# Kernel optimization log

Measured on AMD Instinct MI355X. Metric: run time of the kernel, lower is better.

## Reference

```python
import jax, jax.numpy as jnp
import numpy as np

IN_DIM = 512
HID = 1024
E = 16
TOPK = 2


def setup_inputs() -> dict:
    key = jax.random.key(0)
    ks = jax.random.split(key, 8)
    s = 0.02
    x = jax.random.normal(ks[0], (4, 2048, IN_DIM), dtype=jnp.float32)
    Wr = jax.random.normal(ks[1], (IN_DIM, E), dtype=jnp.float32) * s
    br = jnp.zeros((E,), dtype=jnp.float32)
    W1 = jax.random.normal(ks[2], (E, IN_DIM, HID), dtype=jnp.float32) * s
    b1 = jnp.zeros((E, HID), dtype=jnp.float32)
    W2 = jax.random.normal(ks[3], (E, HID, IN_DIM), dtype=jnp.float32) * s
    b2 = jnp.zeros((E, IN_DIM), dtype=jnp.float32)
    return {"x": x, "Wr": Wr, "br": br, "W1": W1, "b1": b1, "W2": W2, "b2": b2}


def reference(x, Wr, br, W1, b1, W2, b2):
    token_shape = x.shape[:-1]
    xf = x.reshape(-1, x.shape[-1])            # [T, D]
    T = xf.shape[0]

    # router (temperature = 1.0)
    logits = xf @ Wr + br                       # [T, E]
    probs = jax.nn.softmax(logits, axis=-1)
    topk_w, topk_idx = jax.lax.top_k(probs, TOPK)           # [T, K]
    topk_w = topk_w / jnp.maximum(topk_w.sum(-1, keepdims=True), 1e-9)

    # combine weights: [T, E], zero where not routed
    combine = jnp.zeros((T, E), dtype=xf.dtype).at[
        jnp.arange(T)[:, None], topk_idx].add(topk_w)

    # per-expert MLP (exact GELU, as torch nn.GELU default), weighted combine
    y = jnp.zeros_like(xf)
    for e in range(E):
        h = jax.nn.gelu(xf @ W1[e] + b1[e], approximate=False)  # [T, H]
        o = h @ W2[e] + b2[e]                                   # [T, D]
        y = y + combine[:, e:e + 1] * o

    # residual (in_dim == out_dim)
    y = xf + y
    return y.reshape(*token_shape, IN_DIM)
```

## Files before the change

### kernel.cpp

```cpp
#include <hip/hip_runtime.h>
#include <hip/hip_bf16.h>
#include <math.h>

#define IN_DIM 512
#define HID    1024
#define NE     16
#define T_TOK  8192
#define NPAIR  (T_TOK*2)

typedef __attribute__((ext_vector_type(8))) short bf16x8;
typedef __attribute__((ext_vector_type(4))) float f32x4;

__device__ __forceinline__ unsigned short f2b(float f){
  unsigned u = __float_as_uint(f);
  u += 0x7FFF + ((u >> 16) & 1);
  return (unsigned short)(u >> 16);
}
__device__ __forceinline__ float b2f(unsigned short u){
  return __uint_as_float(((unsigned)u) << 16);
}

__device__ __forceinline__ void barrier_lds_only(){
  asm volatile("s_waitcnt lgkmcnt(0)" ::: "memory");
  __builtin_amdgcn_s_barrier();
}

__global__ __launch_bounds__(256) void tconv_kernel(const float* __restrict__ in,
                                                    unsigned short* __restrict__ out,
                                                    int M, int N){
  __shared__ float tile[32][33];
  int e  = blockIdx.z;
  int m0 = blockIdx.y*32, n0 = blockIdx.x*32;
  const float* src = in + (size_t)e*M*N;
  unsigned short* dst = out + (size_t)e*M*N;
  int c = threadIdx.x & 31, r = threadIdx.x >> 5;
  #pragma unroll
  for (int i=0;i<4;i++)
    tile[r + i*8][c] = src[(size_t)(m0 + r + i*8)*N + n0 + c];
  __syncthreads();
  int tr  = threadIdx.x >> 3;
  int tc4 = (threadIdx.x & 7) * 4;
  ushort4 o;
  o.x = f2b(tile[tc4+0][tr]); o.y = f2b(tile[tc4+1][tr]);
  o.z = f2b(tile[tc4+2][tr]); o.w = f2b(tile[tc4+3][tr]);
  *(ushort4*)(&dst[(size_t)(n0 + tr)*M + m0 + tc4]) = o;
}

__global__ __launch_bounds__(256) void router_kernel(
    const float* __restrict__ x, const float* __restrict__ Wr, const float* __restrict__ br,
    unsigned short* __restrict__ xb, int* __restrict__ eid, float* __restrict__ pw)
{
  int wid = threadIdx.x >> 6, lane = threadIdx.x & 63;
  int t = blockIdx.x*4 + wid;
  const float4* xr4 = (const float4*)(x + (size_t)t*IN_DIM);
  ushort4*      xb4 = (ushort4*)(xb + (size_t)t*IN_DIM);

  float acc[NE];
  #pragma unroll
  for (int i=0;i<NE;i++) acc[i]=0.f;

  #pragma unroll
  for (int j=0;j<2;j++){
    int f = j*64 + lane;
    float4 v = xr4[f];
    ushort4 o; o.x=f2b(v.x); o.y=f2b(v.y); o.z=f2b(v.z); o.w=f2b(v.w);
    xb4[f] = o;
    const float4* wr4 = (const float4*)(Wr + (size_t)(f*4)*NE);
    const float* vv = (const float*)&v;
    #pragma unroll
    for (int rr=0; rr<4; rr++){
      float xv = vv[rr];
      #pragma unroll
      for (int q=0;q<4;q++){
        float4 w = wr4[rr*4+q];
        acc[q*4+0] += xv*w.x; acc[q*4+1] += xv*w.y;
        acc[q*4+2] += xv*w.z; acc[q*4+3] += xv*w.w;
      }
    }
  }
  #pragma unroll
  for (int off=32; off>=1; off>>=1){
    #pragma unroll
    for (int i=0;i<NE;i++) acc[i] += __shfl_xor(acc[i], off, 64);
  }
  if (lane==0){
    #pragma unroll
    for (int i=0;i<NE;i++) acc[i] += br[i];
    int e0=0; float l0=acc[0];
    #pragma unroll
    for (int i=1;i<NE;i++) if (acc[i] > l0){ l0=acc[i]; e0=i; }
    int e1=-1; float l1=-3.0e38f;
    #pragma unroll
    for (int i=0;i<NE;i++) if (i!=e0 && acc[i] > l1){ l1=acc[i]; e1=i; }
    float w0 = 1.f/(1.f + __expf(l1 - l0));
    float w1 = 1.f - w0;
    pw[t*2+0] = w0; pw[t*2+1] = w1;
    eid[t*2+0] = e0; eid[t*2+1] = e1;
  }
}

__global__ __launch_bounds__(1024) void bucket_kernel(const int* __restrict__ eid,
                                                      int* __restrict__ cnt,
                                                      int* __restrict__ bucket){
  int e = blockIdx.x;
  __shared__ int lbase;
  if (threadIdx.x == 0) lbase = 0;
  __syncthreads();
  int lane = threadIdx.x & 63, wid = threadIdx.x >> 6;
  int* be = bucket + e*T_TOK;
  for (int c = wid*64; c < NPAIR; c += 1024){
    int p = c + lane;
    bool ok = (eid[p] == e);
    unsigned long long m = __ballot(ok);
    int rank = __popcll(m & ((1ull << lane) - 1ull));
    int count = __popcll(m);
    int base = 0;
    if (lane == 0) base = atomicAdd(&lbase, count);
    base = __shfl(base, 0, 64);
    if (ok) be[base + rank] = p;
  }
  __syncthreads();
  if (threadIdx.x == 0) cnt[e] = lbase;
}

template<int KDIM, int NDIM, bool FIRST>
__global__ __launch_bounds__(256) void moe_gemm(
    const unsigned short* __restrict__ A,
    const unsigned short* __restrict__ Bm,
    const float* __restrict__ bias,
    const int* __restrict__ cnt,
    const int* __restrict__ bucket,
    const float* __restrict__ pw,
    unsigned short* __restrict__ hb,
    unsigned short* __restrict__ opb)
{
  constexpr int NS  = KDIM / 32;
  constexpr int NBT = NDIM / 128;

  int ntiles = 0;
  #pragma unroll
  for (int j=0;j<NE;j++) ntiles += ((cnt[j]+63)>>6)*NBT;

  __shared__ unsigned short As[2*64*32];
  __shared__ unsigned short Bs[2*128*32];

  int tid = threadIdx.x;
  int lane = tid & 63, wid = tid >> 6;
  int wm = (wid>>1)*32, wn = (wid&1)*64;
  int lr0 = tid >> 2;
  int c   = tid & 3;
  int sc  = (c ^ ((lr0 >> 1) & 3)) * 8;
  int wA  = lr0*32 + sc;
  int fr = lane & 15, fb = lane >> 4;
  int pf8 = (fb ^ ((fr >> 1) & 3)) * 8;
  int fq = (lane>>4)*4;

  for (int t = blockIdx.x; t < ntiles; t += gridDim.x){
    int e=0, tloc=0, ebase=0, ce=0, itl=1;
    {
      int cum=0, crow=0;
      #pragma unroll
      for (int j=0;j<NE;j++){
        int cj = cnt[j];
        int it = (cj+63)>>6;
        int tj = it * NBT;
        bool in = (t >= cum) & (t < cum+tj);
        if (in){ e=j; tloc=t-cum; ebase=crow; ce=cj; itl=it; }
        cum += tj; crow += cj;
      }
    }
    int i0 = (tloc % itl) * 64;
    int n0 = (tloc / itl) * 128;

    const int* buck = bucket + e*T_TOK;
    int posA = i0 + lr0;
    int arow;
    if (FIRST){
      int pair = (posA < ce) ? buck[posA] : buck[i0];
      arow = pair >> 1;
    } else {
      arow = ebase + posA;
      if (arow > NPAIR-1) arow = NPAIR-1;
    }
    const unsigned short* Ag = A + (size_t)arow*KDIM + c*8;
    const unsigned short* Bg = Bm + (size_t)e*NDIM*KDIM + (size_t)(n0 + lr0)*KDIM + c*8;

    f32x4 acc[2][4];
    #pragma unroll
    for (int a=0;a<2;a++)
      #pragma unroll
      for (int b=0;b<4;b++)
        #pragma unroll
        for (int j=0;j<4;j++) acc[a][b][j] = 0.f;

    float4 ar, br0, br1;
    ar  = *(const float4*)(Ag);
    br0 = *(const float4*)(Bg);
    br1 = *(const float4*)(Bg + (size_t)64*KDIM);
    *(float4*)(As + wA) = ar;
    *(float4*)(Bs + wA) = br0;
    *(float4*)(Bs + wA + 64*32) = br1;
    ar  = *(const float4*)(Ag + 32);
    br0 = *(const float4*)(Bg + 32);
    br1 = *(const float4*)(Bg + (size_t)64*KDIM + 32);
    barrier_lds_only();

    #pragma unroll 2
    for (int k = 0; k < NS; k++){
      const int cur = k & 1, nxt = cur ^ 1;
      float4 na, nb0, nb1;
      bool ld = (k + 2 < NS);
      if (ld){
        na  = *(const float4*)(Ag + (k+2)*32);
        nb0 = *(const float4*)(Bg + (k+2)*32);
        nb1 = *(const float4*)(Bg + (size_t)64*KDIM + (k+2)*32);
      }
      if (k + 1 < NS){
        *(float4*)(As + nxt*2048 + wA) = ar;
        *(float4*)(Bs + nxt*4096 + wA) = br0;
        *(float4*)(Bs + nxt*4096 + wA + 64*32) = br1;
      }
      if (ld){ ar = na; br0 = nb0; br1 = nb1; }

      const unsigned short* Ac = As + cur*2048;
      const unsigned short* Bc = Bs + cur*4096;
      bf16x8 af[2], bfr[4];
      #pragma unroll
      for (int s=0;s<2;s++) af[s]  = *(const bf16x8*)(Ac + (wm + s*16 + fr)*32 + pf8);
      #pragma unroll
      for (int u=0;u<4;u++) bfr[u] = *(const bf16x8*)(Bc + (wn + u*16 + fr)*32 + pf8);
      #pragma unroll
      for (int s=0;s<2;s++)
        #pragma unroll
        for (int u=0;u<4;u++)
          acc[s][u] = __builtin_amdgcn_mfma_f32_16x16x32_bf16(af[s], bfr[u], acc[s][u], 0,0,0);
      barrier_lds_only();
    }

    #pragma unroll
    for (int s=0;s<2;s++){
      #pragma unroll
      for (int i=0;i<4;i++){
        int row = wm + s*16 + fq + i;
        int pos = i0 + row;
        if (pos >= ce) continue;
        #pragma unroll
        for (int u=0;u<4;u++){
          int n = n0 + wn + u*16 + fr;
          float v = acc[s][u][i] + bias[e*NDIM + n];
          if (FIRST){
            float g = 0.5f*v*(1.f + erff(v*0.70710678118654752f));
            hb[(size_t)(ebase + pos)*NDIM + n] = f2b(g);
          } else {
            int pair = buck[pos];
            opb[(size_t)pair*NDIM + n] = f2b(pw[pair]*v);
          }
        }
      }
    }
  }
}

__global__ __launch_bounds__(256) void combine_kernel(const float* __restrict__ x,
                                                      const unsigned short* __restrict__ opb,
                                                      float* __restrict__ out){
  int i = blockIdx.x*256 + threadIdx.x;
  int t  = i >> 7;
  int c4 = i & 127;
  float4 v = ((const float4*)x)[i];
  ushort4 a = ((const ushort4*)opb)[(size_t)(2*t)*128 + c4];
  ushort4 b = ((const ushort4*)opb)[(size_t)(2*t+1)*128 + c4];
  v.x += b2f(a.x) + b2f(b.x);
  v.y += b2f(a.y) + b2f(b.y);
  v.z += b2f(a.z) + b2f(b.z);
  v.w += b2f(a.w) + b2f(b.w);
  ((float4*)out)[i] = v;
}

extern "C" void kernel_launch(void* const* d_in, const int* in_sizes, int n_in,
                              void* d_out, int out_size, void* d_ws, size_t ws_size,
                              hipStream_t stream)
{
  const float* x  = (const float*)d_in[0];
  const float* Wr = (const float*)d_in[1];
  const float* br = (const float*)d_in[2];
  const float* W1 = (const float*)d_in[3];
  const float* b1 = (const float*)d_in[4];
  const float* W2 = (const float*)d_in[5];
  const float* b2 = (const float*)d_in[6];
  float* out = (float*)d_out;
  char* ws = (char*)d_ws;

  int*            cnt    = (int*)(ws + 0);
  int*            bucket = (int*)(ws + 1024);
  float*          pw     = (float*)(ws + 525312);
  unsigned short* xb     = (unsigned short*)(ws + 590848);
  unsigned short* w1t    = (unsigned short*)(ws + 8979456);
  unsigned short* w2t    = (unsigned short*)(ws + 25756672);
  unsigned short* hb     = (unsigned short*)(ws + 42533888);
  int*            eid    = (int*)(ws + 42533888);
  unsigned short* opb    = w1t;

  router_kernel<<<T_TOK/4, 256, 0, stream>>>(x, Wr, br, xb, eid, pw);
  bucket_kernel<<<NE, 1024, 0, stream>>>(eid, cnt, bucket);
  tconv_kernel<<<dim3(HID/32, IN_DIM/32, NE), 256, 0, stream>>>(W1, w1t, IN_DIM, HID);
  tconv_kernel<<<dim3(IN_DIM/32, HID/32, NE), 256, 0, stream>>>(W2, w2t, HID, IN_DIM);
  moe_gemm<IN_DIM, HID, true ><<<1024, 256, 0, stream>>>(
      xb, w1t, b1, cnt, bucket, pw, hb, opb);
  moe_gemm<HID, IN_DIM, false><<<1024, 256, 0, stream>>>(
      hb, w2t, b2, cnt, bucket, pw, hb, opb);
  combine_kernel<<<(T_TOK*IN_DIM/4)/256, 256, 0, stream>>>(x, opb, out);
}
```

Baseline: 281.3 us.

## Enlarge MoE GEMM tiles to 128x128 with direct global-to-LDS loads

```diff
diff --git a/kernel.cpp b/kernel.cpp
--- a/kernel.cpp
+++ b/kernel.cpp
@@ -25,14 +25,31 @@
   __builtin_amdgcn_s_barrier();
 }
 
-__global__ __launch_bounds__(256) void tconv_kernel(const float* __restrict__ in,
-                                                    unsigned short* __restrict__ out,
-                                                    int M, int N){
+typedef const __attribute__((address_space(1))) unsigned int* gas1_t;
+typedef __attribute__((address_space(3))) unsigned int* las3_t;
+__device__ __forceinline__ void gl16(const unsigned short* g, unsigned short* l){
+  __builtin_amdgcn_global_load_lds((gas1_t)(const void*)g, (las3_t)(void*)l, 16, 0, 0);
+}
+
+__global__ __launch_bounds__(256) void tconv2_kernel(const float* __restrict__ A1,
+                                                     unsigned short* __restrict__ O1,
+                                                     const float* __restrict__ A2,
+                                                     unsigned short* __restrict__ O2){
   __shared__ float tile[32][33];
-  int e  = blockIdx.z;
-  int m0 = blockIdx.y*32, n0 = blockIdx.x*32;
-  const float* src = in + (size_t)e*M*N;
-  unsigned short* dst = out + (size_t)e*M*N;
+  int b = blockIdx.x;
+  const float* src; unsigned short* dst; int M, N, m0, n0;
+  if (b < 8192){
+    M = IN_DIM; N = HID;
+    int e = b >> 9, r = b & 511;
+    n0 = (r & 31)*32; m0 = (r >> 5)*32;
+    src = A1 + (size_t)e*M*N; dst = O1 + (size_t)e*M*N;
+  } else {
+    int b2 = b - 8192;
+    M = HID; N = IN_DIM;
+    int e = b2 >> 9, r = b2 & 511;
+    n0 = (r & 15)*32; m0 = (r >> 4)*32;
+    src = A2 + (size_t)e*M*N; dst = O2 + (size_t)e*M*N;
+  }
   int c = threadIdx.x & 31, r = threadIdx.x >> 5;
   #pragma unroll
   for (int i=0;i<4;i++)
@@ -123,6 +140,37 @@
   if (threadIdx.x == 0) cnt[e] = lbase;
 }
 
+
+#define STAGE(buf, kt) do{ \
+      gl16(Ag0 + (kt)*32, ldsA + (buf)*4096); \
+      gl16(Ag1 + (kt)*32, ldsA + (buf)*4096 + 2048); \
+      gl16(Bg0 + (kt)*32, ldsB + (buf)*4096); \
+      gl16(Bg1 + (kt)*32, ldsB + (buf)*4096 + 2048); \
+    }while(0)
+
+#define COMPUTE(buf) do{ \
+      const unsigned short* Ac = lds + (buf)*4096; \
+      const unsigned short* Bc = lds + 8192 + (buf)*4096; \
+      bf16x8 af[4], bfr[4]; \
+      _Pragma("unroll") \
+      for (int s=0;s<4;s++) af[s]  = *(const bf16x8*)(Ac + (wm + s*16 + fr)*32 + pf8); \
+      _Pragma("unroll") \
+      for (int u=0;u<4;u++) bfr[u] = *(const bf16x8*)(Bc + (wn + u*16 + fr)*32 + pf8); \
+      _Pragma("unroll") \
+      for (int s=0;s<4;s++) \
+        _Pragma("unroll") \
+        for (int u=0;u<4;u++) \
+          acc[s][u] = __builtin_amdgcn_mfma_f32_16x16x32_bf16(af[s], bfr[u], acc[s][u], 0,0,0); \
+    }while(0)
+
+#define KBODY(k, P) do{ \
+      STAGE((P)^1, (k)+1); \
+      asm volatile("s_waitcnt vmcnt(4)" ::: "memory"); \
+      barrier_lds_only(); \
+      COMPUTE(P); \
+      barrier_lds_only(); \
+    }while(0)
+
 template<int KDIM, int NDIM, bool FIRST>
 __global__ __launch_bounds__(256) void moe_gemm(
     const unsigned short* __restrict__ A,
@@ -139,21 +187,22 @@
 
   int ntiles = 0;
   #pragma unroll
-  for (int j=0;j<NE;j++) ntiles += ((cnt[j]+63)>>6)*NBT;
-
-  __shared__ unsigned short As[2*64*32];
-  __shared__ unsigned short Bs[2*128*32];
-
-  int tid = threadIdx.x;
-  int lane = tid & 63, wid = tid >> 6;
-  int wm = (wid>>1)*32, wn = (wid&1)*64;
-  int lr0 = tid >> 2;
-  int c   = tid & 3;
-  int sc  = (c ^ ((lr0 >> 1) & 3)) * 8;
-  int wA  = lr0*32 + sc;
-  int fr = lane & 15, fb = lane >> 4;
-  int pf8 = (fb ^ ((fr >> 1) & 3)) * 8;
-  int fq = (lane>>4)*4;
+  for (int j=0;j<NE;j++) ntiles += ((cnt[j]+127)>>7)*NBT;
+
+  __shared__ unsigned short lds[16384];
+
+  const int tid  = threadIdx.x;
+  const int lane = tid & 63, wid = tid >> 6;
+  const int lr = tid >> 2;
+  const int c  = tid & 3;
+  const int cs = (c ^ ((lr >> 1) & 3)) * 8;
+  unsigned short* ldsA = lds + wid*512;
+  unsigned short* ldsB = lds + 8192 + wid*512;
+
+  const int wm = (wid>>1)*64, wn = (wid&1)*64;
+  const int fr = lane & 15, fb = lane >> 4;
+  const int pf8 = (fb ^ ((fr >> 1) & 3)) * 8;
+  const int fq = fb*4;
 
   for (int t = blockIdx.x; t < ntiles; t += gridDim.x){
     int e=0, tloc=0, ebase=0, ce=0, itl=1;
@@ -162,83 +211,49 @@
       #pragma unroll
       for (int j=0;j<NE;j++){
         int cj = cnt[j];
-        int it = (cj+63)>>6;
+        int it = (cj+127)>>7;
         int tj = it * NBT;
         bool in = (t >= cum) & (t < cum+tj);
         if (in){ e=j; tloc=t-cum; ebase=crow; ce=cj; itl=it; }
         cum += tj; crow += cj;
       }
     }
-    int i0 = (tloc % itl) * 64;
-    int n0 = (tloc / itl) * 128;
+    const int i0 = (tloc % itl) * 128;
+    const int n0 = (tloc / itl) * 128;
 
     const int* buck = bucket + e*T_TOK;
-    int posA = i0 + lr0;
-    int arow;
+    int arow0, arow1;
     if (FIRST){
-      int pair = (posA < ce) ? buck[posA] : buck[i0];
-      arow = pair >> 1;
+      int p0 = i0 + lr, p1 = i0 + 64 + lr;
+      arow0 = buck[(p0 < ce) ? p0 : i0] >> 1;
+      arow1 = buck[(p1 < ce) ? p1 : i0] >> 1;
     } else {
-      arow = ebase + posA;
-      if (arow > NPAIR-1) arow = NPAIR-1;
+      arow0 = ebase + i0 + lr;      if (arow0 > NPAIR-1) arow0 = NPAIR-1;
+      arow1 = ebase + i0 + 64 + lr; if (arow1 > NPAIR-1) arow1 = NPAIR-1;
     }
-    const unsigned short* Ag = A + (size_t)arow*KDIM + c*8;
-    const unsigned short* Bg = Bm + (size_t)e*NDIM*KDIM + (size_t)(n0 + lr0)*KDIM + c*8;
-
-    f32x4 acc[2][4];
-    #pragma unroll
-    for (int a=0;a<2;a++)
+    const unsigned short* Ag0 = A + (size_t)arow0*KDIM + cs;
+    const unsigned short* Ag1 = A + (size_t)arow1*KDIM + cs;
+    const unsigned short* Bg0 = Bm + (size_t)e*NDIM*KDIM + (size_t)(n0 + lr)*KDIM + cs;
+    const unsigned short* Bg1 = Bg0 + (size_t)64*KDIM;
+
+    f32x4 acc[4][4];
+    #pragma unroll
+    for (int s=0;s<4;s++)
       #pragma unroll
-      for (int b=0;b<4;b++)
+      for (int u=0;u<4;u++)
         #pragma unroll
-        for (int j=0;j<4;j++) acc[a][b][j] = 0.f;
-
-    float4 ar, br0, br1;
-    ar  = *(const float4*)(Ag);
-    br0 = *(const float4*)(Bg);
-    br1 = *(const float4*)(Bg + (size_t)64*KDIM);
-    *(float4*)(As + wA) = ar;
-    *(float4*)(Bs + wA) = br0;
-    *(float4*)(Bs + wA + 64*32) = br1;
-    ar  = *(const float4*)(Ag + 32);
-    br0 = *(const float4*)(Bg + 32);
-    br1 = *(const float4*)(Bg + (size_t)64*KDIM + 32);
+        for (int j=0;j<4;j++) acc[s][u][j] = 0.f;
+
+    STAGE(0, 0);
+    for (int k=0; k+1 < NS-1; k+=2){ KBODY(k, 0); KBODY(k+1, 1); }
+    KBODY(NS-2, 0);
+    asm volatile("s_waitcnt vmcnt(0)" ::: "memory");
     barrier_lds_only();
-
-    #pragma unroll 2
-    for (int k = 0; k < NS; k++){
-      const int cur = k & 1, nxt = cur ^ 1;
-      float4 na, nb0, nb1;
-      bool ld = (k + 2 < NS);
-      if (ld){
-        na  = *(const float4*)(Ag + (k+2)*32);
-        nb0 = *(const float4*)(Bg + (k+2)*32);
-        nb1 = *(const float4*)(Bg + (size_t)64*KDIM + (k+2)*32);
-      }
-      if (k + 1 < NS){
-        *(float4*)(As + nxt*2048 + wA) = ar;
-        *(float4*)(Bs + nxt*4096 + wA) = br0;
-        *(float4*)(Bs + nxt*4096 + wA + 64*32) = br1;
-      }
-      if (ld){ ar = na; br0 = nb0; br1 = nb1; }
-
-      const unsigned short* Ac = As + cur*2048;
-      const unsigned short* Bc = Bs + cur*4096;
-      bf16x8 af[2], bfr[4];
-      #pragma unroll
-      for (int s=0;s<2;s++) af[s]  = *(const bf16x8*)(Ac + (wm + s*16 + fr)*32 + pf8);
-      #pragma unroll
-      for (int u=0;u<4;u++) bfr[u] = *(const bf16x8*)(Bc + (wn + u*16 + fr)*32 + pf8);
-      #pragma unroll
-      for (int s=0;s<2;s++)
-        #pragma unroll
-        for (int u=0;u<4;u++)
-          acc[s][u] = __builtin_amdgcn_mfma_f32_16x16x32_bf16(af[s], bfr[u], acc[s][u], 0,0,0);
-      barrier_lds_only();
-    }
-
-    #pragma unroll
-    for (int s=0;s<2;s++){
+    COMPUTE(1);
+    barrier_lds_only();
+
+    #pragma unroll
+    for (int s=0;s<4;s++){
       #pragma unroll
       for (int i=0;i<4;i++){
         int row = wm + s*16 + fq + i;
@@ -261,6 +276,10 @@
   }
 }
 
+#undef KBODY
+#undef COMPUTE
+#undef STAGE
+
 __global__ __launch_bounds__(256) void combine_kernel(const float* __restrict__ x,
                                                       const unsigned short* __restrict__ opb,
                                                       float* __restrict__ out){
@@ -303,8 +322,7 @@
 
   router_kernel<<<T_TOK/4, 256, 0, stream>>>(x, Wr, br, xb, eid, pw);
   bucket_kernel<<<NE, 1024, 0, stream>>>(eid, cnt, bucket);
-  tconv_kernel<<<dim3(HID/32, IN_DIM/32, NE), 256, 0, stream>>>(W1, w1t, IN_DIM, HID);
-  tconv_kernel<<<dim3(IN_DIM/32, HID/32, NE), 256, 0, stream>>>(W2, w2t, HID, IN_DIM);
+  tconv2_kernel<<<16384, 256, 0, stream>>>(W1, w1t, W2, w2t);
   moe_gemm<IN_DIM, HID, true ><<<1024, 256, 0, stream>>>(
       xb, w1t, b1, cnt, bucket, pw, hb, opb);
   moe_gemm<HID, IN_DIM, false><<<1024, 256, 0, stream>>>(
```

Result: no change. 286.7 us (+1.9%).

## Use 128x128 tiles for first expert GEMM and merge weight transposes

Applied to the files above, without the earlier changes.

```diff
diff --git a/kernel.cpp b/kernel.cpp
--- a/kernel.cpp
+++ b/kernel.cpp
@@ -25,14 +25,25 @@
   __builtin_amdgcn_s_barrier();
 }
 
-__global__ __launch_bounds__(256) void tconv_kernel(const float* __restrict__ in,
-                                                    unsigned short* __restrict__ out,
-                                                    int M, int N){
+__global__ __launch_bounds__(256) void tconv2_kernel(const float* __restrict__ A1,
+                                                     unsigned short* __restrict__ O1,
+                                                     const float* __restrict__ A2,
+                                                     unsigned short* __restrict__ O2){
   __shared__ float tile[32][33];
-  int e  = blockIdx.z;
-  int m0 = blockIdx.y*32, n0 = blockIdx.x*32;
-  const float* src = in + (size_t)e*M*N;
-  unsigned short* dst = out + (size_t)e*M*N;
+  int b = blockIdx.x;
+  const float* src; unsigned short* dst; int M, N, m0, n0;
+  if (b < 8192){
+    M = IN_DIM; N = HID;
+    int e = b >> 9, r = b & 511;
+    n0 = (r & 31)*32; m0 = (r >> 5)*32;
+    src = A1 + (size_t)e*M*N; dst = O1 + (size_t)e*M*N;
+  } else {
+    int b2 = b - 8192;
+    M = HID; N = IN_DIM;
+    int e = b2 >> 9, r = b2 & 511;
+    n0 = (r & 15)*32; m0 = (r >> 4)*32;
+    src = A2 + (size_t)e*M*N; dst = O2 + (size_t)e*M*N;
+  }
   int c = threadIdx.x & 31, r = threadIdx.x >> 5;
   #pragma unroll
   for (int i=0;i<4;i++)
@@ -124,6 +135,154 @@
 }
 
 template<int KDIM, int NDIM, bool FIRST>
+__global__ __launch_bounds__(256) void moe_gemm128(
+    const unsigned short* __restrict__ A,
+    const unsigned short* __restrict__ Bm,
+    const float* __restrict__ bias,
+    const int* __restrict__ cnt,
+    const int* __restrict__ bucket,
+    const float* __restrict__ pw,
+    unsigned short* __restrict__ hb,
+    unsigned short* __restrict__ opb)
+{
+  constexpr int NS  = KDIM / 32;
+  constexpr int NBT = NDIM / 128;
+
+  int ntiles = 0;
+  #pragma unroll
+  for (int j=0;j<NE;j++) ntiles += ((cnt[j]+127)>>7)*NBT;
+
+  __shared__ unsigned short As[2*128*32];
+  __shared__ unsigned short Bs[2*128*32];
+
+  const int tid  = threadIdx.x;
+  const int lane = tid & 63, wid = tid >> 6;
+  const int lr0 = tid >> 2;
+  const int c   = tid & 3;
+  const int sc  = (c ^ ((lr0 >> 1) & 3)) * 8;
+  const int wA  = lr0*32 + sc;
+  const int fr = lane & 15, fb = lane >> 4;
+  const int pf8 = (fb ^ ((fr >> 1) & 3)) * 8;
+  const int fq = fb*4;
+  const int wm = (wid>>1)*64, wn = (wid&1)*64;
+
+  const int t0 = (blockIdx.x & 7)*128 + (blockIdx.x >> 3);
+  for (int t = t0; t < ntiles; t += gridDim.x){
+    int e=0, tloc=0, ebase=0, ce=0, itl=1;
+    {
+      int cum=0, crow=0;
+      #pragma unroll
+      for (int j=0;j<NE;j++){
+        int cj = cnt[j];
+        int it = (cj+127)>>7;
+        int tj = it * NBT;
+        bool in = (t >= cum) & (t < cum+tj);
+        if (in){ e=j; tloc=t-cum; ebase=crow; ce=cj; itl=it; }
+        cum += tj; crow += cj;
+      }
+    }
+    const int i0 = (tloc % itl) * 128;
+    const int n0 = (tloc / itl) * 128;
+
+    const int* buck = bucket + e*T_TOK;
+    int p0 = i0 + lr0, p1 = p0 + 64;
+    int ar0, ar1;
+    if (FIRST){
+      ar0 = buck[(p0 < ce) ? p0 : i0] >> 1;
+      ar1 = buck[(p1 < ce) ? p1 : i0] >> 1;
+    } else {
+      ar0 = ebase + p0; if (ar0 > NPAIR-1) ar0 = NPAIR-1;
+      ar1 = ebase + p1; if (ar1 > NPAIR-1) ar1 = NPAIR-1;
+    }
+    const unsigned short* Ag0 = A + (size_t)ar0*KDIM + c*8;
+    const unsigned short* Ag1 = A + (size_t)ar1*KDIM + c*8;
+    const unsigned short* Bg0 = Bm + (size_t)e*NDIM*KDIM + (size_t)(n0 + lr0)*KDIM + c*8;
+    const unsigned short* Bg1 = Bg0 + (size_t)64*KDIM;
+
+    f32x4 acc[4][4];
+    #pragma unroll
+    for (int s=0;s<4;s++)
+      #pragma unroll
+      for (int u=0;u<4;u++)
+        #pragma unroll
+        for (int j=0;j<4;j++) acc[s][u][j] = 0.f;
+
+    float4 a0,a1,b0,b1;
+    a0 = *(const float4*)(Ag0);
+    a1 = *(const float4*)(Ag1);
+    b0 = *(const float4*)(Bg0);
+    b1 = *(const float4*)(Bg1);
+    *(float4*)(As + wA) = a0;
+    *(float4*)(As + wA + 64*32) = a1;
+    *(float4*)(Bs + wA) = b0;
+    *(float4*)(Bs + wA + 64*32) = b1;
+    a0 = *(const float4*)(Ag0 + 32);
+    a1 = *(const float4*)(Ag1 + 32);
+    b0 = *(const float4*)(Bg0 + 32);
+    b1 = *(const float4*)(Bg1 + 32);
+    barrier_lds_only();
+
+    #pragma unroll 2
+    for (int k = 0; k < NS; k++){
+      const int cur = k & 1, nxt = cur ^ 1;
+      float4 na0,na1,nb0,nb1;
+      bool ld = (k + 2 < NS);
+      if (ld){
+        na0 = *(const float4*)(Ag0 + (k+2)*32);
+        na1 = *(const float4*)(Ag1 + (k+2)*32);
+        nb0 = *(const float4*)(Bg0 + (k+2)*32);
+        nb1 = *(const float4*)(Bg1 + (k+2)*32);
+      }
+      if (k + 1 < NS){
+        *(float4*)(As + nxt*4096 + wA) = a0;
+        *(float4*)(As + nxt*4096 + wA + 64*32) = a1;
+        *(float4*)(Bs + nxt*4096 + wA) = b0;
+        *(float4*)(Bs + nxt*4096 + wA + 64*32) = b1;
+      }
+      if (ld){ a0=na0; a1=na1; b0=nb0; b1=nb1; }
+
+      const unsigned short* Ac = As + cur*4096;
+      const unsigned short* Bc = Bs + cur*4096;
+      bf16x8 af[4], bfr[4];
+      #pragma unroll
+      for (int s=0;s<4;s++) af[s]  = *(const bf16x8*)(Ac + (wm + s*16 + fr)*32 + pf8);
+      #pragma unroll
+      for (int u=0;u<4;u++) bfr[u] = *(const bf16x8*)(Bc + (wn + u*16 + fr)*32 + pf8);
+      #pragma unroll
+      for (int s=0;s<4;s++)
+        #pragma unroll
+        for (int u=0;u<4;u++)
+          acc[s][u] = __builtin_amdgcn_mfma_f32_16x16x32_bf16(af[s], bfr[u], acc[s][u], 0,0,0);
+      barrier_lds_only();
+    }
+
+    const float* be = bias + e*NDIM;
+    #pragma unroll
+    for (int s=0;s<4;s++){
+      #pragma unroll
+      for (int i=0;i<4;i++){
+        int row = wm + s*16 + fq + i;
+        int pos = i0 + row;
+        if (pos >= ce) continue;
+        int pair = 0; float pwv = 0.f;
+        if (!FIRST){ pair = buck[pos]; pwv = pw[pair]; }
+        #pragma unroll
+        for (int u=0;u<4;u++){
+          int n = n0 + wn + u*16 + fr;
+          float v = acc[s][u][i] + be[n];
+          if (FIRST){
+            float g = 0.5f*v*(1.f + erff(v*0.70710678118654752f));
+            hb[(size_t)(ebase + pos)*NDIM + n] = f2b(g);
+          } else {
+            opb[(size_t)pair*NDIM + n] = f2b(pwv*v);
+          }
+        }
+      }
+    }
+  }
+}
+
+template<int KDIM, int NDIM, bool FIRST>
 __global__ __launch_bounds__(256) void moe_gemm(
     const unsigned short* __restrict__ A,
     const unsigned short* __restrict__ Bm,
@@ -303,9 +462,8 @@
 
   router_kernel<<<T_TOK/4, 256, 0, stream>>>(x, Wr, br, xb, eid, pw);
   bucket_kernel<<<NE, 1024, 0, stream>>>(eid, cnt, bucket);
-  tconv_kernel<<<dim3(HID/32, IN_DIM/32, NE), 256, 0, stream>>>(W1, w1t, IN_DIM, HID);
-  tconv_kernel<<<dim3(IN_DIM/32, HID/32, NE), 256, 0, stream>>>(W2, w2t, HID, IN_DIM);
-  moe_gemm<IN_DIM, HID, true ><<<1024, 256, 0, stream>>>(
+  tconv2_kernel<<<16384, 256, 0, stream>>>(W1, w1t, W2, w2t);
+  moe_gemm128<IN_DIM, HID, true ><<<1024, 256, 0, stream>>>(
       xb, w1t, b1, cnt, bucket, pw, hb, opb);
   moe_gemm<HID, IN_DIM, false><<<1024, 256, 0, stream>>>(
       hb, w2t, b2, cnt, bucket, pw, hb, opb);
```

Result: slower. 293.4 us (+4.3%).
